# Kernel tuning notes

Measured on AMD Instinct MI355X. Metric: run time of the kernel, lower is better.

Reference implementation:

```python
import jax, jax.numpy as jnp
import numpy as np

EPS = 1e-12  # F.normalize eps


def _l2norm(v, axis):
    n = jnp.sqrt(jnp.sum(v * v, axis=axis, keepdims=True))
    return v / jnp.maximum(n, EPS)


def setup_inputs() -> dict:
    key = jax.random.key(0)
    k1, k2, k3, k4 = jax.random.split(key, 4)
    N, C, H, W = 48, 512, 40, 40
    K = 64
    x = jax.random.normal(k1, (N, C, H, W), dtype=jnp.float32)
    conv_w = jax.random.normal(k2, (K, C), dtype=jnp.float32) * 0.02   # cluster-assign 1x1 conv, no bias (vladv2=False)
    attn_w = jax.random.normal(k3, (1, C), dtype=jnp.float32) * 0.02   # heatmap 1x1 conv
    attn_b = jnp.zeros((1,), dtype=jnp.float32)
    centroids = jax.random.uniform(k4, (K, C), dtype=jnp.float32)      # torch.rand init
    return {"x": x, "conv_w": conv_w, "attn_w": attn_w, "attn_b": attn_b, "centroids": centroids}


def reference(x, conv_w, attn_w, attn_b, centroids):
    N, C, H, W = x.shape
    K = conv_w.shape[0]
    P = H * W

    # attention heatmap: ReLU -> 1x1 conv -> ReLU  => [N, 1, H, W]
    hmp = jax.nn.relu(jnp.einsum('nchw,oc->nohw', jax.nn.relu(x), attn_w) + attn_b[None, :, None, None])
    hmp_flat = hmp.reshape(N, 1, P)  # [N,1,P]

    # normalize input descriptors across channels
    xn = _l2norm(x, axis=1)                      # [N,C,H,W]
    x_flat = xn.reshape(N, C, P)                 # [N,C,P]

    # soft assignment: 1x1 conv over clusters + softmax over cluster dim
    logits = jnp.einsum('ncp,kc->nkp', x_flat, conv_w)   # [N,K,P]
    soft_assign = jax.nn.softmax(logits, axis=1)          # softmax over K

    # weighted residual aggregation, fused:
    # vlad[n,k,c] = sum_p (x[n,c,p] - centroids[k,c]) * sa[n,k,p] * hmp[n,0,p]
    w = soft_assign * hmp_flat                            # [N,K,P]
    term1 = jnp.einsum('nkp,ncp->nkc', w, x_flat)         # [N,K,C]
    wsum = jnp.sum(w, axis=-1)                            # [N,K]
    vlad = term1 - wsum[:, :, None] * centroids[None, :, :]

    vlad = _l2norm(vlad, axis=2)                          # intra-normalize per cluster
    vlad = vlad.reshape(N, K * C)
    vlad = _l2norm(vlad, axis=1)                          # global L2 normalize
    return vlad
```

## Files before the change

### kernel.cpp

```cpp
#include <hip/hip_runtime.h>
#include <math.h>

#define NN 48
#define CC 512
#define KK 64
#define PP 1600
#define EPSF 1e-12f

typedef short short8 __attribute__((ext_vector_type(8)));
typedef float f32x4 __attribute__((ext_vector_type(4)));

static __device__ __forceinline__ unsigned short f2bf(float f) {
    unsigned u = __float_as_uint(f);
    u += 0x7fffu + ((u >> 16) & 1u);
    return (unsigned short)(u >> 16);
}
static __device__ __forceinline__ unsigned pack2(float a, float b) {
    return (unsigned)f2bf(a) | ((unsigned)f2bf(b) << 16);
}

__global__ __launch_bounds__(256) void kn_logits(
    const float* __restrict__ x, const float* __restrict__ conv_w,
    const float* __restrict__ attn_w, const float* __restrict__ attn_b,
    unsigned short* __restrict__ wg, float* __restrict__ wsum,
    unsigned short* __restrict__ xbf)
{
    __shared__ unsigned short xt[64][140];
    __shared__ unsigned short cwb[64][72];
    __shared__ float attn_l[CC];
    __shared__ float red[8][128];
    __shared__ float invn_l[128];
    __shared__ float hmp_l[128];

    const int n = blockIdx.y, p0 = blockIdx.x * 128, tid = threadIdx.x;
    const int q = tid & 31, cg8 = tid >> 5;
    const int wave = tid >> 6, lane = tid & 63;
    const int lq = lane >> 4, lm = lane & 15;
    const bool pval = (p0 + q * 4) < PP;

    for (int i = tid; i < CC; i += 256) attn_l[i] = attn_w[i];

    f32x4 acc[4][2];
#pragma unroll
    for (int mt = 0; mt < 4; ++mt)
#pragma unroll
        for (int nt = 0; nt < 2; ++nt) acc[mt][nt] = (f32x4){0.f, 0.f, 0.f, 0.f};
    float ss[4] = {0.f, 0.f, 0.f, 0.f};
    float ad[4] = {0.f, 0.f, 0.f, 0.f};

    const float* xb = x + (size_t)n * CC * PP;
    __syncthreads();

    for (int cs = 0; cs < 8; ++cs) {
        const int c0 = cs * 64;
        {
            const int kr = tid >> 2, cq = tid & 3;
            const float* wp = conv_w + kr * CC + c0 + cq * 16;
#pragma unroll
            for (int j = 0; j < 4; ++j) {
                float4 v = *(const float4*)(wp + 4 * j);
                uint2 u = {pack2(v.x, v.y), pack2(v.z, v.w)};
                *(uint2*)&cwb[kr][cq * 16 + 4 * j] = u;
            }
        }
#pragma unroll
        for (int j = 0; j < 8; ++j) {
            const int cl = cg8 * 8 + j, cg = c0 + cl;
            float4 v = make_float4(0.f, 0.f, 0.f, 0.f);
            if (pval) v = *(const float4*)(xb + (size_t)cg * PP + p0 + 4 * q);
            const float aw = attn_l[cg];
            ss[0] += v.x * v.x; ss[1] += v.y * v.y;
            ss[2] += v.z * v.z; ss[3] += v.w * v.w;
            ad[0] += fmaxf(v.x, 0.f) * aw; ad[1] += fmaxf(v.y, 0.f) * aw;
            ad[2] += fmaxf(v.z, 0.f) * aw; ad[3] += fmaxf(v.w, 0.f) * aw;
            uint2 u = {pack2(v.x, v.y), pack2(v.z, v.w)};
            *(uint2*)&xt[cl][4 * q] = u;
            if (xbf && pval)
                *(uint2*)(xbf + ((size_t)n * CC + cg) * PP + p0 + 4 * q) = u;
        }
        __syncthreads();
#pragma unroll
        for (int ks = 0; ks < 2; ++ks) {
            short8 af[4];
#pragma unroll
            for (int mt = 0; mt < 4; ++mt)
                af[mt] = *(const short8*)&cwb[mt * 16 + lm][ks * 32 + lq * 8];
#pragma unroll
            for (int nt = 0; nt < 2; ++nt) {
                const int pl = wave * 32 + nt * 16 + lm;
                const int cb = ks * 32 + lq * 8;
                short8 bv;
#pragma unroll
                for (int j = 0; j < 8; ++j) bv[j] = (short)xt[cb + j][pl];
#pragma unroll
                for (int mt = 0; mt < 4; ++mt)
                    acc[mt][nt] = __builtin_amdgcn_mfma_f32_16x16x32_bf16(
                        af[mt], bv, acc[mt][nt], 0, 0, 0);
            }
        }
        __syncthreads();
    }

#pragma unroll
    for (int j = 0; j < 4; ++j) red[cg8][q * 4 + j] = ss[j];
    __syncthreads();
    if (tid < 128) {
        float S = 0.f;
#pragma unroll
        for (int l = 0; l < 8; ++l) S += red[l][tid];
        invn_l[tid] = 1.f / fmaxf(sqrtf(S), EPSF);
    }
    __syncthreads();
#pragma unroll
    for (int j = 0; j < 4; ++j) red[cg8][q * 4 + j] = ad[j];
    __syncthreads();
    if (tid < 128) {
        float A = 0.f;
#pragma unroll
        for (int l = 0; l < 8; ++l) A += red[l][tid];
        hmp_l[tid] = fmaxf(A + attn_b[0], 0.f);
    }
    __syncthreads();

    float invv[2], sden[2];
#pragma unroll
    for (int nt = 0; nt < 2; ++nt) {
        const int pl = wave * 32 + nt * 16 + lm;
        const bool pv = (p0 + pl) < PP;
        const float inv = invn_l[pl];
        const float hp = pv ? hmp_l[pl] : 0.f;
        float mx = -1e30f;
#pragma unroll
        for (int mt = 0; mt < 4; ++mt)
#pragma unroll
            for (int r = 0; r < 4; ++r) {
                const float l = acc[mt][nt][r] * inv;
                acc[mt][nt][r] = l;
                mx = fmaxf(mx, l);
            }
        mx = fmaxf(mx, __shfl_xor(mx, 16));
        mx = fmaxf(mx, __shfl_xor(mx, 32));
        float s = 0.f;
#pragma unroll
        for (int mt = 0; mt < 4; ++mt)
#pragma unroll
            for (int r = 0; r < 4; ++r) {
                const float e = __expf(acc[mt][nt][r] - mx);
                acc[mt][nt][r] = e;
                s += e;
            }
        s += __shfl_xor(s, 16);
        s += __shfl_xor(s, 32);
        sden[nt] = hp / s;
        invv[nt] = inv;
    }

    const int pl0 = wave * 32 + lm, pl1 = pl0 + 16;
    const bool v0 = (p0 + pl0) < PP, v1 = (p0 + pl1) < PP;
#pragma unroll
    for (int mt = 0; mt < 4; ++mt)
#pragma unroll
        for (int r = 0; r < 4; ++r) {
            const int k = mt * 16 + lq * 4 + r;
            const float w0 = acc[mt][0][r] * sden[0];
            const float w1 = acc[mt][1][r] * sden[1];
            float wk = w0 + w1;
#pragma unroll
            for (int o = 1; o < 16; o <<= 1) wk += __shfl_xor(wk, o);
            if (lm == 0) atomicAdd(&wsum[n * KK + k], wk);
            unsigned short* wr = wg + ((size_t)n * KK + k) * PP + p0;
            if (v0) wr[pl0] = f2bf(w0 * invv[0]);
            if (v1) wr[pl1] = f2bf(w1 * invv[1]);
        }
}

template <bool XB>
__global__ __launch_bounds__(256) void kn_term1(
    const float* __restrict__ xf, const unsigned short* __restrict__ xbf,
    const unsigned short* __restrict__ wgq, float* __restrict__ term1p)
{
    __shared__ unsigned short wt[64][40];
    __shared__ unsigned short xt2[128][40];
    const int c0 = blockIdx.x * 128, n = blockIdx.y, ph = blockIdx.z;
    const int tid = threadIdx.x;
    const int wave = tid >> 6, lane = tid & 63, lq = lane >> 4, lm = lane & 15;
    const int koff = (wave >> 1) * 32, coff = (wave & 1) * 64;
    const int s_begin = (50 * ph) >> 2, s_end = (50 * (ph + 1)) >> 2;

    const int rA = tid >> 2, cqA = tid & 3;
    const int rB0 = tid >> 2, cqB0 = tid & 3;
    const int rB1 = (256 + tid) >> 2, cqB1 = tid & 3;

    f32x4 acc[2][4];
#pragma unroll
    for (int mt = 0; mt < 2; ++mt)
#pragma unroll
        for (int nt = 0; nt < 4; ++nt) acc[mt][nt] = (f32x4){0.f, 0.f, 0.f, 0.f};

    const unsigned short* wb = wgq + (size_t)n * KK * PP;

    auto ldA = [&](int p0) -> uint4 {
        return *(const uint4*)(wb + (size_t)rA * PP + p0 + cqA * 8);
    };
    auto ldB = [&](int p0, int row, int cq) -> uint4 {
        if (XB) {
            return *(const uint4*)(xbf + ((size_t)n * CC + c0 + row) * PP + p0 + cq * 8);
        } else {
            const float* sp = xf + ((size_t)n * CC + c0 + row) * PP + p0 + cq * 8;
            float4 a = *(const float4*)sp, b = *(const float4*)(sp + 4);
            return make_uint4(pack2(a.x, a.y), pack2(a.z, a.w),
                              pack2(b.x, b.y), pack2(b.z, b.w));
        }
    };

    uint4 pa = ldA(s_begin * 32);
    uint4 pb0 = ldB(s_begin * 32, rB0, cqB0);
    uint4 pb1 = ldB(s_begin * 32, rB1, cqB1);

    for (int ps = s_begin; ps < s_end; ++ps) {
        *(uint4*)&wt[rA][cqA * 8] = pa;
        *(uint4*)&xt2[rB0][cqB0 * 8] = pb0;
        *(uint4*)&xt2[rB1][cqB1 * 8] = pb1;
        __syncthreads();
        uint4 na, nb0, nb1;
        if (ps + 1 < s_end) {
            const int p1 = (ps + 1) * 32;
            na = ldA(p1); nb0 = ldB(p1, rB0, cqB0); nb1 = ldB(p1, rB1, cqB1);
        }
        short8 af[2], bv[4];
#pragma unroll
        for (int mt = 0; mt < 2; ++mt)
            af[mt] = *(const short8*)&wt[koff + mt * 16 + lm][lq * 8];
#pragma unroll
        for (int nt = 0; nt < 4; ++nt)
            bv[nt] = *(const short8*)&xt2[coff + nt * 16 + lm][lq * 8];
#pragma unroll
        for (int mt = 0; mt < 2; ++mt)
#pragma unroll
            for (int nt = 0; nt < 4; ++nt)
                acc[mt][nt] = __builtin_amdgcn_mfma_f32_16x16x32_bf16(
                    af[mt], bv[nt], acc[mt][nt], 0, 0, 0);
        __syncthreads();
        pa = na; pb0 = nb0; pb1 = nb1;
    }

    float* ob = term1p + ((size_t)ph * NN + n) * KK * CC;
#pragma unroll
    for (int mt = 0; mt < 2; ++mt)
#pragma unroll
        for (int r = 0; r < 4; ++r) {
            const int k = koff + mt * 16 + lq * 4 + r;
#pragma unroll
            for (int nt = 0; nt < 4; ++nt)
                ob[(size_t)k * CC + c0 + coff + nt * 16 + lm] = acc[mt][nt][r];
        }
}

__global__ __launch_bounds__(128) void kn_vlad(
    const float* __restrict__ term1p, const float* __restrict__ wsum,
    const float* __restrict__ cent, float* __restrict__ out,
    float* __restrict__ nsum)
{
    const int k = blockIdx.x, n = blockIdx.y, tid = threadIdx.x;
    const size_t base = ((size_t)n * KK + k) * CC;
    const size_t NKC = (size_t)NN * KK * CC;
    const float ws = wsum[n * KK + k];
    const int c = tid * 4;

    float4 ce = *(const float4*)(cent + (size_t)k * CC + c);
    float4 v = {-ws * ce.x, -ws * ce.y, -ws * ce.z, -ws * ce.w};
#pragma unroll
    for (int h = 0; h < 4; ++h) {
        float4 a = *(const float4*)(term1p + h * NKC + base + c);
        v.x += a.x; v.y += a.y; v.z += a.z; v.w += a.w;
    }

    float s = v.x * v.x + v.y * v.y + v.z * v.z + v.w * v.w;
#pragma unroll
    for (int o = 32; o >= 1; o >>= 1) s += __shfl_down(s, o, 64);

    __shared__ float rb[2];
    __shared__ float sinv;
    if ((tid & 63) == 0) rb[tid >> 6] = s;
    __syncthreads();
    if (tid == 0) {
        const float S = rb[0] + rb[1];
        const float inv = 1.f / fmaxf(sqrtf(S), EPSF);
        sinv = inv;
        atomicAdd(&nsum[n], S * inv * inv);
    }
    __syncthreads();
    const float inv = sinv;
    float4 o4 = {v.x * inv, v.y * inv, v.z * inv, v.w * inv};
    *(float4*)(out + base + c) = o4;
}

__global__ __launch_bounds__(256) void kn_scale(
    float* __restrict__ out, const float* __restrict__ nsum)
{
    const int n = blockIdx.y;
    const size_t off = ((size_t)blockIdx.x * 256 + threadIdx.x) * 4;
    const float g = 1.f / fmaxf(sqrtf(nsum[n]), EPSF);
    float4 v = *(float4*)(out + (size_t)n * KK * CC + off);
    v.x *= g; v.y *= g; v.z *= g; v.w *= g;
    *(float4*)(out + (size_t)n * KK * CC + off) = v;
}

extern "C" void kernel_launch(void* const* d_in, const int* in_sizes, int n_in,
                              void* d_out, int out_size, void* d_ws, size_t ws_size,
                              hipStream_t stream)
{
    (void)in_sizes; (void)n_in; (void)out_size;
    const float* x      = (const float*)d_in[0];
    const float* conv_w = (const float*)d_in[1];
    const float* attn_w = (const float*)d_in[2];
    const float* attn_b = (const float*)d_in[3];
    const float* cent   = (const float*)d_in[4];
    float* out = (float*)d_out;

    char* w = (char*)d_ws;
    float* term1p = (float*)w;            w += (size_t)4 * NN * KK * CC * 4;
    float* wsum   = (float*)w;            w += (size_t)NN * KK * 4;
    float* nsum   = (float*)w;            w += 256;
    unsigned short* wg  = (unsigned short*)w; w += (size_t)NN * KK * PP * 2;
    unsigned short* xbf = (unsigned short*)w;
    const size_t need_xb = (size_t)(w - (char*)d_ws) + (size_t)NN * CC * PP * 2;
    const bool xb = ws_size >= need_xb;

    hipMemsetAsync(wsum, 0, NN * KK * sizeof(float), stream);
    hipMemsetAsync(nsum, 0, NN * sizeof(float), stream);

    kn_logits<<<dim3(13, NN), 256, 0, stream>>>(x, conv_w, attn_w, attn_b,
                                                wg, wsum, xb ? xbf : nullptr);
    if (xb)
        kn_term1<true><<<dim3(4, NN, 4), 256, 0, stream>>>(x, xbf, wg, term1p);
    else
        kn_term1<false><<<dim3(4, NN, 4), 256, 0, stream>>>(x, xbf, wg, term1p);
    kn_vlad <<<dim3(KK, NN), 128, 0, stream>>>(term1p, wsum, cent, out, nsum);
    kn_scale<<<dim3(32, NN), 256, 0, stream>>>(out, nsum);
}
```

Baseline: 318.4 us.

## Halve logits tile to 64 pixels and double-buffer global loads in registers

The logits kernel now covers 64 pixels per block instead of 128, so the grid grows from 13 to 25 blocks per image, and the partial tail tile and its bounds checks are gone because 1600 divides evenly by 64. The next channel slice of x and conv_w is prefetched into registers while the MFMA work on the current slice runs, hiding global-load latency. The aim is better occupancy and less load stall in the first kernel, since the old grid was small and partly idle. The cost is that each block re-converts conv_w for a smaller pixel tile, and the extra prefetch registers raise register pressure.

```diff
diff --git a/kernel.cpp b/kernel.cpp
--- a/kernel.cpp
+++ b/kernel.cpp
@@ -25,152 +25,138 @@
     unsigned short* __restrict__ wg, float* __restrict__ wsum,
     unsigned short* __restrict__ xbf)
 {
-    __shared__ unsigned short xt[64][140];
+    __shared__ unsigned short xt[64][68];
     __shared__ unsigned short cwb[64][72];
     __shared__ float attn_l[CC];
-    __shared__ float red[8][128];
-    __shared__ float invn_l[128];
-    __shared__ float hmp_l[128];
-
-    const int n = blockIdx.y, p0 = blockIdx.x * 128, tid = threadIdx.x;
-    const int q = tid & 31, cg8 = tid >> 5;
+    __shared__ float red[16][66];
+    __shared__ float invn_l[64];
+    __shared__ float hmp_l[64];
+
+    const int n = blockIdx.y, p0 = blockIdx.x * 64, tid = threadIdx.x;
+    const int pq = tid & 15, crow = tid >> 4;
+    const int kr = tid >> 2, cq = tid & 3;
     const int wave = tid >> 6, lane = tid & 63;
     const int lq = lane >> 4, lm = lane & 15;
-    const bool pval = (p0 + q * 4) < PP;
+    const int pw = wave * 16 + lm;
 
     for (int i = tid; i < CC; i += 256) attn_l[i] = attn_w[i];
 
-    f32x4 acc[4][2];
-#pragma unroll
-    for (int mt = 0; mt < 4; ++mt)
-#pragma unroll
-        for (int nt = 0; nt < 2; ++nt) acc[mt][nt] = (f32x4){0.f, 0.f, 0.f, 0.f};
+    f32x4 acc[4];
+#pragma unroll
+    for (int mt = 0; mt < 4; ++mt) acc[mt] = (f32x4){0.f, 0.f, 0.f, 0.f};
     float ss[4] = {0.f, 0.f, 0.f, 0.f};
     float ad[4] = {0.f, 0.f, 0.f, 0.f};
 
-    const float* xb = x + (size_t)n * CC * PP;
+    const float* xb = x + (size_t)n * CC * PP + p0;
+
+    float4 xr[2][4], wr4[2][4];
+#pragma unroll
+    for (int j = 0; j < 4; ++j) {
+        xr[0][j]  = *(const float4*)(xb + (size_t)(crow + 16 * j) * PP + 4 * pq);
+        wr4[0][j] = *(const float4*)(conv_w + kr * CC + cq * 16 + 4 * j);
+    }
     __syncthreads();
 
     for (int cs = 0; cs < 8; ++cs) {
-        const int c0 = cs * 64;
-        {
-            const int kr = tid >> 2, cq = tid & 3;
-            const float* wp = conv_w + kr * CC + c0 + cq * 16;
-#pragma unroll
-            for (int j = 0; j < 4; ++j) {
-                float4 v = *(const float4*)(wp + 4 * j);
-                uint2 u = {pack2(v.x, v.y), pack2(v.z, v.w)};
-                *(uint2*)&cwb[kr][cq * 16 + 4 * j] = u;
-            }
-        }
-#pragma unroll
-        for (int j = 0; j < 8; ++j) {
-            const int cl = cg8 * 8 + j, cg = c0 + cl;
-            float4 v = make_float4(0.f, 0.f, 0.f, 0.f);
-            if (pval) v = *(const float4*)(xb + (size_t)cg * PP + p0 + 4 * q);
-            const float aw = attn_l[cg];
+        const int cur = cs & 1, nxt = cur ^ 1, c0 = cs * 64;
+#pragma unroll
+        for (int j = 0; j < 4; ++j) {
+            const int cl = crow + 16 * j;
+            const float4 v = xr[cur][j];
+            const float aw = attn_l[c0 + cl];
             ss[0] += v.x * v.x; ss[1] += v.y * v.y;
             ss[2] += v.z * v.z; ss[3] += v.w * v.w;
             ad[0] += fmaxf(v.x, 0.f) * aw; ad[1] += fmaxf(v.y, 0.f) * aw;
             ad[2] += fmaxf(v.z, 0.f) * aw; ad[3] += fmaxf(v.w, 0.f) * aw;
-            uint2 u = {pack2(v.x, v.y), pack2(v.z, v.w)};
-            *(uint2*)&xt[cl][4 * q] = u;
-            if (xbf && pval)
-                *(uint2*)(xbf + ((size_t)n * CC + cg) * PP + p0 + 4 * q) = u;
+            const uint2 u = {pack2(v.x, v.y), pack2(v.z, v.w)};
+            *(uint2*)&xt[cl][4 * pq] = u;
+            if (xbf)
+                *(uint2*)(xbf + ((size_t)n * CC + c0 + cl) * PP + p0 + 4 * pq) = u;
+            const float4 w4 = wr4[cur][j];
+            const uint2 uw = {pack2(w4.x, w4.y), pack2(w4.z, w4.w)};
+            *(uint2*)&cwb[kr][cq * 16 + 4 * j] = uw;
         }
         __syncthreads();
+        if (cs < 7) {
+            const int c1 = c0 + 64;
+#pragma unroll
+            for (int j = 0; j < 4; ++j) {
+                xr[nxt][j]  = *(const float4*)(xb + (size_t)(c1 + crow + 16 * j) * PP + 4 * pq);
+                wr4[nxt][j] = *(const float4*)(conv_w + kr * CC + c1 + cq * 16 + 4 * j);
+            }
+        }
 #pragma unroll
         for (int ks = 0; ks < 2; ++ks) {
-            short8 af[4];
-#pragma unroll
-            for (int mt = 0; mt < 4; ++mt)
-                af[mt] = *(const short8*)&cwb[mt * 16 + lm][ks * 32 + lq * 8];
-#pragma unroll
-            for (int nt = 0; nt < 2; ++nt) {
-                const int pl = wave * 32 + nt * 16 + lm;
-                const int cb = ks * 32 + lq * 8;
-                short8 bv;
-#pragma unroll
-                for (int j = 0; j < 8; ++j) bv[j] = (short)xt[cb + j][pl];
-#pragma unroll
-                for (int mt = 0; mt < 4; ++mt)
-                    acc[mt][nt] = __builtin_amdgcn_mfma_f32_16x16x32_bf16(
-                        af[mt], bv, acc[mt][nt], 0, 0, 0);
+            short8 bv;
+#pragma unroll
+            for (int j = 0; j < 8; ++j) bv[j] = (short)xt[ks * 32 + lq * 8 + j][pw];
+#pragma unroll
+            for (int mt = 0; mt < 4; ++mt) {
+                const short8 af = *(const short8*)&cwb[mt * 16 + lm][ks * 32 + lq * 8];
+                acc[mt] = __builtin_amdgcn_mfma_f32_16x16x32_bf16(af, bv, acc[mt], 0, 0, 0);
             }
         }
         __syncthreads();
     }
 
 #pragma unroll
-    for (int j = 0; j < 4; ++j) red[cg8][q * 4 + j] = ss[j];
-    __syncthreads();
-    if (tid < 128) {
+    for (int j = 0; j < 4; ++j) red[crow][4 * pq + j] = ss[j];
+    __syncthreads();
+    if (tid < 64) {
         float S = 0.f;
 #pragma unroll
-        for (int l = 0; l < 8; ++l) S += red[l][tid];
+        for (int l = 0; l < 16; ++l) S += red[l][tid];
         invn_l[tid] = 1.f / fmaxf(sqrtf(S), EPSF);
     }
     __syncthreads();
 #pragma unroll
-    for (int j = 0; j < 4; ++j) red[cg8][q * 4 + j] = ad[j];
-    __syncthreads();
-    if (tid < 128) {
+    for (int j = 0; j < 4; ++j) red[crow][4 * pq + j] = ad[j];
+    __syncthreads();
+    if (tid < 64) {
         float A = 0.f;
 #pragma unroll
-        for (int l = 0; l < 8; ++l) A += red[l][tid];
+        for (int l = 0; l < 16; ++l) A += red[l][tid];
         hmp_l[tid] = fmaxf(A + attn_b[0], 0.f);
     }
     __syncthreads();
 
-    float invv[2], sden[2];
-#pragma unroll
-    for (int nt = 0; nt < 2; ++nt) {
-        const int pl = wave * 32 + nt * 16 + lm;
-        const bool pv = (p0 + pl) < PP;
-        const float inv = invn_l[pl];
-        const float hp = pv ? hmp_l[pl] : 0.f;
-        float mx = -1e30f;
-#pragma unroll
-        for (int mt = 0; mt < 4; ++mt)
-#pragma unroll
-            for (int r = 0; r < 4; ++r) {
-                const float l = acc[mt][nt][r] * inv;
-                acc[mt][nt][r] = l;
-                mx = fmaxf(mx, l);
-            }
-        mx = fmaxf(mx, __shfl_xor(mx, 16));
-        mx = fmaxf(mx, __shfl_xor(mx, 32));
-        float s = 0.f;
-#pragma unroll
-        for (int mt = 0; mt < 4; ++mt)
-#pragma unroll
-            for (int r = 0; r < 4; ++r) {
-                const float e = __expf(acc[mt][nt][r] - mx);
-                acc[mt][nt][r] = e;
-                s += e;
-            }
-        s += __shfl_xor(s, 16);
-        s += __shfl_xor(s, 32);
-        sden[nt] = hp / s;
-        invv[nt] = inv;
-    }
-
-    const int pl0 = wave * 32 + lm, pl1 = pl0 + 16;
-    const bool v0 = (p0 + pl0) < PP, v1 = (p0 + pl1) < PP;
+    const float inv = invn_l[pw];
+    const float hp  = hmp_l[pw];
+    float mx = -1e30f;
 #pragma unroll
     for (int mt = 0; mt < 4; ++mt)
 #pragma unroll
         for (int r = 0; r < 4; ++r) {
+            const float l = acc[mt][r] * inv;
+            acc[mt][r] = l;
+            mx = fmaxf(mx, l);
+        }
+    mx = fmaxf(mx, __shfl_xor(mx, 16));
+    mx = fmaxf(mx, __shfl_xor(mx, 32));
+    float s = 0.f;
+#pragma unroll
+    for (int mt = 0; mt < 4; ++mt)
+#pragma unroll
+        for (int r = 0; r < 4; ++r) {
+            const float e = __expf(acc[mt][r] - mx);
+            acc[mt][r] = e;
+            s += e;
+        }
+    s += __shfl_xor(s, 16);
+    s += __shfl_xor(s, 32);
+    const float sden = hp / s;
+
+#pragma unroll
+    for (int mt = 0; mt < 4; ++mt)
+#pragma unroll
+        for (int r = 0; r < 4; ++r) {
+            const float w = acc[mt][r] * sden;
+            float wk = w;
+#pragma unroll
+            for (int o = 1; o < 16; o <<= 1) wk += __shfl_xor(wk, o);
             const int k = mt * 16 + lq * 4 + r;
-            const float w0 = acc[mt][0][r] * sden[0];
-            const float w1 = acc[mt][1][r] * sden[1];
-            float wk = w0 + w1;
-#pragma unroll
-            for (int o = 1; o < 16; o <<= 1) wk += __shfl_xor(wk, o);
             if (lm == 0) atomicAdd(&wsum[n * KK + k], wk);
-            unsigned short* wr = wg + ((size_t)n * KK + k) * PP + p0;
-            if (v0) wr[pl0] = f2bf(w0 * invv[0]);
-            if (v1) wr[pl1] = f2bf(w1 * invv[1]);
+            wg[((size_t)n * KK + k) * PP + p0 + pw] = f2bf(w * inv);
         }
 }
 
@@ -330,7 +316,7 @@
     hipMemsetAsync(wsum, 0, NN * KK * sizeof(float), stream);
     hipMemsetAsync(nsum, 0, NN * sizeof(float), stream);
 
-    kn_logits<<<dim3(13, NN), 256, 0, stream>>>(x, conv_w, attn_w, attn_b,
+    kn_logits<<<dim3(25, NN), 256, 0, stream>>>(x, conv_w, attn_w, attn_b,
                                                 wg, wsum, xb ? xbf : nullptr);
     if (xb)
         kn_term1<true><<<dim3(4, NN, 4), 256, 0, stream>>>(x, xbf, wg, term1p);
```

New measurement: 435.4 us. 36.7% more time.
